# Kernel tuning notes

Measured on AMD Instinct MI355X. Metric: run time of the kernel, lower is better.

## Reference

```python
import jax, jax.numpy as jnp
import numpy as np

B, N, E, H, MAXLEN = 64, 256, 1024, 16, 512
D = E // H
LN_EPS = 1e-5
NORM_EPS = 1e-12


def setup_inputs() -> dict:
    key = jax.random.key(0)
    ks = jax.random.split(key, 12)
    s = 1.0 / np.sqrt(E)
    return {
        "news_embeds": jax.random.normal(ks[0], (B, N, E), jnp.float32),
        "padding_mask": jax.random.uniform(ks[1], (B, N)) > 0.8,  # True = padded
        "cls_token": jax.random.normal(ks[2], (1, 1, E), jnp.float32),
        "pos_emb": jax.random.normal(ks[3], (MAXLEN + 1, E), jnp.float32) * 0.02,
        "in_proj_w": jax.random.normal(ks[4], (3 * E, E), jnp.float32) * s,
        "in_proj_b": jnp.zeros((3 * E,), jnp.float32),
        "out_proj_w": jax.random.normal(ks[5], (E, E), jnp.float32) * s,
        "out_proj_b": jnp.zeros((E,), jnp.float32),
        "proj_w": jax.random.normal(ks[6], (E, E), jnp.float32) * s,
        "proj_b": jnp.zeros((E,), jnp.float32),
        "ln_gamma": jnp.ones((E,), jnp.float32),
        "ln_beta": jnp.zeros((E,), jnp.float32),
    }


def reference(news_embeds, padding_mask, cls_token, pos_emb, in_proj_w, in_proj_b,
              out_proj_w, out_proj_b, proj_w, proj_b, ln_gamma, ln_beta):
    b, n, e = news_embeds.shape
    S = n + 1
    # prepend CLS token, add positional encodings (dropout inactive in eval)
    x = jnp.concatenate([jnp.broadcast_to(cls_token, (b, 1, e)), news_embeds], axis=1)
    x = x + pos_emb[:S][None, :, :]
    # key padding mask with CLS always attendable
    mask = jnp.concatenate(
        [jnp.zeros((b, 1), dtype=bool), padding_mask], axis=1)  # [b,S]
    # packed QKV projection (nn.MultiheadAttention in_proj)
    qkv = jnp.einsum('bse,fe->bsf', x, in_proj_w) + in_proj_b
    q, k, v = jnp.split(qkv, 3, axis=-1)
    q = q.reshape(b, S, H, D)
    k = k.reshape(b, S, H, D)
    v = v.reshape(b, S, H, D)
    scores = jnp.einsum('bqhd,bkhd->bhqk', q, k) / jnp.sqrt(
        jnp.asarray(D, x.dtype))
    big_neg = jnp.asarray(-1e9, scores.dtype)
    scores = jnp.where(mask[:, None, None, :], big_neg, scores)
    attn = jax.nn.softmax(scores, axis=-1)  # [b,H,S,S]
    ctx = jnp.einsum('bhqk,bkhd->bqhd', attn, v).reshape(b, S, e)
    attn_out = jnp.einsum('bse,fe->bsf', ctx, out_proj_w) + out_proj_b
    # projection head: Linear -> (Dropout eval noop) -> LayerNorm -> ReLU
    p = jnp.einsum('bse,fe->bsf', attn_out, proj_w) + proj_b
    mu = jnp.mean(p, axis=-1, keepdims=True)
    var = jnp.var(p, axis=-1, keepdims=True)
    ln = (p - mu) * jax.lax.rsqrt(var + LN_EPS) * ln_gamma + ln_beta
    proj = jax.nn.relu(ln)
    user = proj[:, 0, :]
    norm = jnp.maximum(jnp.linalg.norm(user, axis=-1, keepdims=True), NORM_EPS)
    user = user / norm
    return user, attn
```

## Files before the change

kernel.cpp:

```cpp
#include <hip/hip_runtime.h>

#define B_   64
#define N_   256
#define E_   1024
#define H_   16
#define D_   64
#define S_   257
#define M_   16448
#define MP2  16640
#define N3_  3072
#define K_   1024

typedef unsigned short u16;
typedef unsigned int   u32;
typedef __bf16 bf16x8 __attribute__((ext_vector_type(8)));
typedef float  f32x4  __attribute__((ext_vector_type(4)));

__device__ inline u16 f2bf(float f) {
  union { float f; u32 u; } a; a.f = f;
  return (u16)((a.u + 0x7FFFu + ((a.u >> 16) & 1u)) >> 16);
}
__device__ inline float bf2f(u16 h) {
  union { u32 u; float f; } a; a.u = ((u32)h) << 16; return a.f;
}
__device__ inline void gload_lds16(const void* g, void* l) {
  __builtin_amdgcn_global_load_lds((const __attribute__((address_space(1))) void*)g,
                                   (__attribute__((address_space(3))) void*)l, 16, 0, 0);
}

__global__ __launch_bounds__(256) void prep_w(const float* __restrict__ w, u16* __restrict__ o) {
  size_t i = ((size_t)blockIdx.x * 256 + threadIdx.x) * 4;
  float4 f = *(const float4*)(w + i);
  ushort4 v;
  v.x = f2bf(f.x); v.y = f2bf(f.y); v.z = f2bf(f.z); v.w = f2bf(f.w);
  *(ushort4*)(o + i) = v;
}

__global__ __launch_bounds__(256) void build_x(const float* __restrict__ news,
                                               const float* __restrict__ cls,
                                               const float* __restrict__ pos,
                                               u16* __restrict__ x) {
  const int row = blockIdx.x;
  const int e = threadIdx.x * 4;
  float4 v = make_float4(0.f, 0.f, 0.f, 0.f);
  if (row < M_) {
    const int b = row / S_;
    const int s = row - b * S_;
    float4 pe = *(const float4*)(pos + (size_t)s * E_ + e);
    float4 xv = (s == 0) ? *(const float4*)(cls + e)
                         : *(const float4*)(news + ((size_t)b * N_ + (s - 1)) * E_ + e);
    v.x = xv.x + pe.x; v.y = xv.y + pe.y; v.z = xv.z + pe.z; v.w = xv.w + pe.w;
  }
  ushort4 o;
  o.x = f2bf(v.x); o.y = f2bf(v.y); o.z = f2bf(v.z); o.w = f2bf(v.w);
  *(ushort4*)(x + (size_t)row * E_ + e) = o;
}

__global__ __launch_bounds__(256) void mask_prep(const void* __restrict__ src, int* __restrict__ dst) {
  const int t = threadIdx.x;
  const u32* wsrc = (const u32*)src;
  u32 flag = 0;
  for (int i = t; i < 4096; i += 256) {
    u32 v = wsrc[i];
    if (v == 0x3F800000u) flag |= 2u;
    else if (v > 1u) flag |= 1u;
  }
  __shared__ u32 fsh;
  if (t == 0) fsh = 0;
  __syncthreads();
  if (flag) atomicOr(&fsh, flag);
  __syncthreads();
  const u32 f = fsh;
  const int mode = (f & 2u) ? 2 : ((f & 1u) ? 1 : 0);
  const int base = blockIdx.x * 2048;
  for (int i = base + t; i < base + 2048; i += 256) {
    int m;
    if (mode == 0)      m = (wsrc[i] != 0u);
    else if (mode == 2) m = (((const float*)src)[i] != 0.f);
    else                m = (((const unsigned char*)src)[i] != 0);
    dst[i] = m;
  }
}

__global__ __launch_bounds__(256) void gemm_qkv(const u16* __restrict__ A,
                                                const u16* __restrict__ Bw,
                                                const float* __restrict__ bias,
                                                u16* __restrict__ C) {
  __shared__ u16 As[128 * 32];
  __shared__ u16 Bs[128 * 32];
  const int t = threadIdx.x;
  const int w = t >> 6, l = t & 63;
  const int wr = w >> 1, wc = w & 1;

  const int orig = blockIdx.x;
  const int wgid = (orig & 7) * 390 + (orig >> 3);
  const int bm = wgid / 24, bn = wgid % 24;

  const u16* Ab = A + (size_t)bm * 128 * K_;
  const u16* Bb = Bw + (size_t)bn * 128 * K_;
  f32x4 acc[4][4] = {};
  const int r0 = t >> 2,         col0 = (t & 3) << 3;
  const int r1 = (256 + t) >> 2, col1 = ((256 + t) & 3) << 3;
  char* AsB = (char*)As + w * 1024;
  char* BsB = (char*)Bs + w * 1024;

  for (int k0 = 0; k0 < K_; k0 += 32) {
    gload_lds16(Ab + (size_t)r0 * K_ + k0 + col0, AsB);
    gload_lds16(Ab + (size_t)r1 * K_ + k0 + col1, AsB + 4096);
    gload_lds16(Bb + (size_t)r0 * K_ + k0 + col0, BsB);
    gload_lds16(Bb + (size_t)r1 * K_ + k0 + col1, BsB + 4096);
    __syncthreads();
    const int kc = (l >> 4) << 3;
    bf16x8 af[4], bfr[4];
#pragma unroll
    for (int m = 0; m < 4; ++m)
      af[m] = *(const bf16x8*)&As[(wr * 64 + m * 16 + (l & 15)) * 32 + kc];
#pragma unroll
    for (int n = 0; n < 4; ++n)
      bfr[n] = *(const bf16x8*)&Bs[(wc * 64 + n * 16 + (l & 15)) * 32 + kc];
#pragma unroll
    for (int m = 0; m < 4; ++m)
#pragma unroll
      for (int n = 0; n < 4; ++n)
        acc[m][n] = __builtin_amdgcn_mfma_f32_16x16x32_bf16(af[m], bfr[n], acc[m][n], 0, 0, 0);
    __syncthreads();
  }
  const int row0 = bm * 128 + wr * 64 + ((l >> 4) << 2);
  const int colb = bn * 128 + wc * 64 + (l & 15);
#pragma unroll
  for (int n = 0; n < 4; ++n) {
    const int col = colb + n * 16;
    const float bv = bias[col];
#pragma unroll
    for (int m = 0; m < 4; ++m) {
      const int row = row0 + m * 16;
#pragma unroll
      for (int j = 0; j < 4; ++j)
        C[(size_t)(row + j) * N3_ + col] = f2bf(acc[m][n][j] + bv);
    }
  }
}

__global__ __launch_bounds__(256) void attn_kernel(const u16* __restrict__ qkv,
                                                   const int* __restrict__ maskw,
                                                   float* __restrict__ attn,
                                                   float* __restrict__ ctx) {
  __shared__ u16 Ks[258 * 72];
  __shared__ float msk[272];
  __shared__ float p0[272];
  __shared__ float red[4][64];
  const int qt = blockIdx.x, h = blockIdx.y, b = blockIdx.z;
  const int t = threadIdx.x;
  const int q0 = qt * 64;

  for (int c = t; c < 258 * 8; c += 256) {
    const int r = c >> 3, qq = c & 7;
    uint4 val = make_uint4(0, 0, 0, 0);
    if (r < S_)
      val = *(const uint4*)(qkv + (size_t)(b * S_ + r) * N3_ + E_ + h * 64 + qq * 8);
    *(uint4*)&Ks[r * 72 + qq * 8] = val;
  }
  for (int i = t; i < 272; i += 256) {
    float m = 0.f;
    if (i == 0) m = 1.f;
    else if (i < S_) m = maskw[b * N_ + i - 1] ? 0.f : 1.f;
    msk[i] = m;
  }
  __syncthreads();

  const int w = t >> 6, l = t & 63;
  const int cl = l & 15, rg = l >> 4;
  const int kc = rg * 8;

  const u16* qrow = qkv + (size_t)(b * S_ + q0 + w * 16 + cl) * N3_ + h * 64 + kc;
  const bf16x8 qa0 = *(const bf16x8*)qrow;
  const bf16x8 qa1 = *(const bf16x8*)(qrow + 32);

#define QK(kt, a)                                                                  \
  {                                                                                \
    int krow = (kt) * 16 + cl;                                                     \
    if (krow > 257) krow = 257;                                                    \
    const u16* kb = &Ks[krow * 72 + kc];                                           \
    (a) = __builtin_amdgcn_mfma_f32_16x16x32_bf16(qa0, *(const bf16x8*)kb, (a), 0, 0, 0); \
    (a) = __builtin_amdgcn_mfma_f32_16x16x32_bf16(qa1, *(const bf16x8*)(kb + 32), (a), 0, 0, 0); \
  }

  float sum[4] = {0.f, 0.f, 0.f, 0.f};
#pragma unroll
  for (int kt = 0; kt < 17; ++kt) {
    f32x4 a = {0.f, 0.f, 0.f, 0.f};
    QK(kt, a);
    const float m = msk[kt * 16 + cl];
#pragma unroll
    for (int j = 0; j < 4; ++j)
      sum[j] += m * __expf(a[j] * 0.125f);
  }
  float inv[4];
#pragma unroll
  for (int j = 0; j < 4; ++j) {
#pragma unroll
    for (int o = 1; o < 16; o <<= 1) sum[j] += __shfl_xor(sum[j], o);
    inv[j] = 1.f / sum[j];
  }

  const int qrow0 = q0 + w * 16 + rg * 4;
  float* abase = attn + (size_t)(b * H_ + h) * S_ * S_;
  float* arow[4];
  bool okq[4];
#pragma unroll
  for (int j = 0; j < 4; ++j) {
    const int gq = qrow0 + j;
    okq[j] = (gq < S_);
    arow[j] = abase + (size_t)gq * S_;
  }
  const bool isCls = (qt == 0 && w == 0 && rg == 0);
#pragma unroll
  for (int kt = 0; kt < 17; ++kt) {
    f32x4 a = {0.f, 0.f, 0.f, 0.f};
    QK(kt, a);
    const float m = msk[kt * 16 + cl];
    const int col = kt * 16 + cl;
    const bool okc = (col < S_);
#pragma unroll
    for (int j = 0; j < 4; ++j) {
      const float v = m * __expf(a[j] * 0.125f) * inv[j];
      if (okc && okq[j]) arow[j][col] = v;
      if (isCls && j == 0) p0[col] = v;
    }
  }
#undef QK

  if (qt == 0) {
    __syncthreads();
    const int part = t >> 6, d = t & 63;
    float acc = 0.f;
    for (int k = part; k < S_; k += 4)
      acc = fmaf(p0[k], bf2f(qkv[(size_t)(b * S_ + k) * N3_ + 2 * E_ + h * 64 + d]), acc);
    red[part][d] = acc;
    __syncthreads();
    if (t < 64)
      ctx[(size_t)b * E_ + h * 64 + t] = red[0][t] + red[1][t] + red[2][t] + red[3][t];
  }
}

__global__ __launch_bounds__(256) void gemv_cls(const float* __restrict__ in,
                                                const float* __restrict__ W,
                                                const float* __restrict__ bias,
                                                float* __restrict__ out) {
  const int bt = blockIdx.x, fc = blockIdx.y, t = threadIdx.x;
  __shared__ float xs[4][E_];
  for (int i = t; i < E_; i += 256)
    ((float4*)xs)[i] = ((const float4*)(in + (size_t)bt * 4 * E_))[i];
  __syncthreads();
  const int f = fc * 64 + (t >> 2);
  const int ec = (t & 3) * 256;
  const float4* wr = (const float4*)(W + (size_t)f * E_ + ec);
  float a0 = 0.f, a1 = 0.f, a2 = 0.f, a3 = 0.f;
#pragma unroll 8
  for (int e4 = 0; e4 < 64; ++e4) {
    const float4 wv = wr[e4];
    const float4 x0 = *(const float4*)&xs[0][ec + e4 * 4];
    const float4 x1 = *(const float4*)&xs[1][ec + e4 * 4];
    const float4 x2 = *(const float4*)&xs[2][ec + e4 * 4];
    const float4 x3 = *(const float4*)&xs[3][ec + e4 * 4];
    a0 += wv.x * x0.x + wv.y * x0.y + wv.z * x0.z + wv.w * x0.w;
    a1 += wv.x * x1.x + wv.y * x1.y + wv.z * x1.z + wv.w * x1.w;
    a2 += wv.x * x2.x + wv.y * x2.y + wv.z * x2.z + wv.w * x2.w;
    a3 += wv.x * x3.x + wv.y * x3.y + wv.z * x3.z + wv.w * x3.w;
  }
  a0 += __shfl_xor(a0, 1); a0 += __shfl_xor(a0, 2);
  a1 += __shfl_xor(a1, 1); a1 += __shfl_xor(a1, 2);
  a2 += __shfl_xor(a2, 1); a2 += __shfl_xor(a2, 2);
  a3 += __shfl_xor(a3, 1); a3 += __shfl_xor(a3, 2);
  if ((t & 3) == 0) {
    const float bv = bias[f];
    out[(size_t)(bt * 4 + 0) * E_ + f] = a0 + bv;
    out[(size_t)(bt * 4 + 1) * E_ + f] = a1 + bv;
    out[(size_t)(bt * 4 + 2) * E_ + f] = a2 + bv;
    out[(size_t)(bt * 4 + 3) * E_ + f] = a3 + bv;
  }
}

__global__ __launch_bounds__(256) void ln_relu_norm(const float* __restrict__ p,
                                                    const float* __restrict__ gamma,
                                                    const float* __restrict__ beta,
                                                    float* __restrict__ user) {
  const int b = blockIdx.x, t = threadIdx.x;
  const int w = t >> 6, l = t & 63;
  const float4 v = ((const float4*)(p + (size_t)b * E_))[t];
  float s = v.x + v.y + v.z + v.w;
  float s2 = v.x * v.x + v.y * v.y + v.z * v.z + v.w * v.w;
#pragma unroll
  for (int o = 1; o < 64; o <<= 1) { s += __shfl_xor(s, o); s2 += __shfl_xor(s2, o); }
  __shared__ float ss[4], ss2[4], qs[4];
  if (l == 0) { ss[w] = s; ss2[w] = s2; }
  __syncthreads();
  s = ss[0] + ss[1] + ss[2] + ss[3];
  s2 = ss2[0] + ss2[1] + ss2[2] + ss2[3];
  const float mu = s * (1.f / E_);
  const float var = s2 * (1.f / E_) - mu * mu;
  const float rstd = rsqrtf(var + 1e-5f);
  const float4 g = ((const float4*)gamma)[t];
  const float4 be = ((const float4*)beta)[t];
  float4 o;
  o.x = fmaxf((v.x - mu) * rstd * g.x + be.x, 0.f);
  o.y = fmaxf((v.y - mu) * rstd * g.y + be.y, 0.f);
  o.z = fmaxf((v.z - mu) * rstd * g.z + be.z, 0.f);
  o.w = fmaxf((v.w - mu) * rstd * g.w + be.w, 0.f);
  float q2 = o.x * o.x + o.y * o.y + o.z * o.z + o.w * o.w;
#pragma unroll
  for (int off = 1; off < 64; off <<= 1) q2 += __shfl_xor(q2, off);
  if (l == 0) qs[w] = q2;
  __syncthreads();
  q2 = qs[0] + qs[1] + qs[2] + qs[3];
  const float nrm = fmaxf(sqrtf(q2), 1e-12f);
  const float inv = 1.f / nrm;
  float4 u;
  u.x = o.x * inv; u.y = o.y * inv; u.z = o.z * inv; u.w = o.w * inv;
  ((float4*)(user + (size_t)b * E_))[t] = u;
}

extern "C" void kernel_launch(void* const* d_in, const int* in_sizes, int n_in,
                              void* d_out, int out_size, void* d_ws, size_t ws_size,
                              hipStream_t stream) {
  const float* news   = (const float*)d_in[0];
  const void*  maskp  = d_in[1];
  const float* cls    = (const float*)d_in[2];
  const float* pos    = (const float*)d_in[3];
  const float* w_in   = (const float*)d_in[4];
  const float* b_in   = (const float*)d_in[5];
  const float* w_out  = (const float*)d_in[6];
  const float* b_out  = (const float*)d_in[7];
  const float* w_proj = (const float*)d_in[8];
  const float* b_proj = (const float*)d_in[9];
  const float* gamma  = (const float*)d_in[10];
  const float* beta   = (const float*)d_in[11];

  char* ws = (char*)d_ws;
  u16*  w_bf  = (u16*)(ws + 0);
  u16*  x_bf  = (u16*)(ws + 6291456);
  u16*  qkv   = (u16*)(ws + 40370176);
  float* ctx  = (float*)(ws + 142606336);
  float* aoc  = (float*)(ws + 142868480);
  float* pcls = (float*)(ws + 143130624);
  int*  maskw = (int*)(ws + 143392768);

  float* user = (float*)d_out;
  float* attn = (float*)d_out + (size_t)B_ * E_;

  prep_w<<<3072, 256, 0, stream>>>(w_in, w_bf);
  build_x<<<MP2, 256, 0, stream>>>(news, cls, pos, x_bf);
  mask_prep<<<8, 256, 0, stream>>>(maskp, maskw);
  gemm_qkv<<<3120, 256, 0, stream>>>(x_bf, w_bf, b_in, qkv);
  attn_kernel<<<dim3(5, H_, B_), 256, 0, stream>>>(qkv, maskw, attn, ctx);
  gemv_cls<<<dim3(16, 16), 256, 0, stream>>>(ctx, w_out, b_out, aoc);
  gemv_cls<<<dim3(16, 16), 256, 0, stream>>>(aoc, w_proj, b_proj, pcls);
  ln_relu_norm<<<B_, 256, 0, stream>>>(pcls, gamma, beta, user);
}
```

Measured before the change: 357.8 us.

## Use fragment-ordered LDS staging in QKV GEMM and transpose attention score MFMA

The QKV GEMM now stages 64-wide K slices per barrier, laid out in LDS so each lane reads its MFMA fragment contiguously. This halves the barrier count and avoids bank conflicts. The attention kernel swaps the MFMA operands so each lane holds four consecutive key columns of one query row. That reduces the row-sum to two shuffles and allows 16-byte vector stores of attention probabilities instead of scattered scalar stores. The stores are only 4-byte aligned because S=257 is odd, so memcpy may split them, and the doubled LDS footprint may lower occupancy.

```diff
diff --git a/kernel.cpp b/kernel.cpp
--- a/kernel.cpp
+++ b/kernel.cpp
@@ -86,8 +86,8 @@
                                                 const u16* __restrict__ Bw,
                                                 const float* __restrict__ bias,
                                                 u16* __restrict__ C) {
-  __shared__ u16 As[128 * 32];
-  __shared__ u16 Bs[128 * 32];
+  __shared__ u16 ldsA[8192];
+  __shared__ u16 ldsB[8192];
   const int t = threadIdx.x;
   const int w = t >> 6, l = t & 63;
   const int wr = w >> 1, wc = w & 1;
@@ -96,35 +96,45 @@
   const int wgid = (orig & 7) * 390 + (orig >> 3);
   const int bm = wgid / 24, bn = wgid % 24;
 
-  const u16* Ab = A + (size_t)bm * 128 * K_;
-  const u16* Bb = Bw + (size_t)bn * 128 * K_;
+  const u16* Abase = A + (size_t)bm * 128 * K_;
+  const u16* Bbase = Bw + (size_t)bn * 128 * K_;
+
   f32x4 acc[4][4] = {};
-  const int r0 = t >> 2,         col0 = (t & 3) << 3;
-  const int r1 = (256 + t) >> 2, col1 = ((256 + t) & 3) << 3;
-  char* AsB = (char*)As + w * 1024;
-  char* BsB = (char*)Bs + w * 1024;
-
-  for (int k0 = 0; k0 < K_; k0 += 32) {
-    gload_lds16(Ab + (size_t)r0 * K_ + k0 + col0, AsB);
-    gload_lds16(Ab + (size_t)r1 * K_ + k0 + col1, AsB + 4096);
-    gload_lds16(Bb + (size_t)r0 * K_ + k0 + col0, BsB);
-    gload_lds16(Bb + (size_t)r1 * K_ + k0 + col1, BsB + 4096);
+
+#define STAGE(k0)                                                                 \
+  {                                                                               \
+    _Pragma("unroll")                                                             \
+    for (int c = 0; c < 4; ++c) {                                                 \
+      const int bi = w * 4 + c;                                                   \
+      const size_t off = (size_t)((bi >> 1) * 16 + (l & 15)) * K_ +               \
+                         (bi & 1) * 32 + ((l >> 4) * 8) + (k0);                   \
+      gload_lds16(Abase + off, (char*)ldsA + bi * 1024);                          \
+      gload_lds16(Bbase + off, (char*)ldsB + bi * 1024);                          \
+    }                                                                             \
+  }
+
+  for (int kt = 0; kt < 16; ++kt) {
+    STAGE(kt * 64);
     __syncthreads();
-    const int kc = (l >> 4) << 3;
-    bf16x8 af[4], bfr[4];
-#pragma unroll
-    for (int m = 0; m < 4; ++m)
-      af[m] = *(const bf16x8*)&As[(wr * 64 + m * 16 + (l & 15)) * 32 + kc];
-#pragma unroll
-    for (int n = 0; n < 4; ++n)
-      bfr[n] = *(const bf16x8*)&Bs[(wc * 64 + n * 16 + (l & 15)) * 32 + kc];
-#pragma unroll
-    for (int m = 0; m < 4; ++m)
+#pragma unroll
+    for (int half = 0; half < 2; ++half) {
+      bf16x8 af[4], bfx[4];
+#pragma unroll
+      for (int m = 0; m < 4; ++m)
+        af[m] = *(const bf16x8*)&ldsA[(((wr * 4 + m) * 2 + half) * 64 + l) * 8];
 #pragma unroll
       for (int n = 0; n < 4; ++n)
-        acc[m][n] = __builtin_amdgcn_mfma_f32_16x16x32_bf16(af[m], bfr[n], acc[m][n], 0, 0, 0);
+        bfx[n] = *(const bf16x8*)&ldsB[(((wc * 4 + n) * 2 + half) * 64 + l) * 8];
+#pragma unroll
+      for (int m = 0; m < 4; ++m)
+#pragma unroll
+        for (int n = 0; n < 4; ++n)
+          acc[m][n] = __builtin_amdgcn_mfma_f32_16x16x32_bf16(af[m], bfx[n], acc[m][n], 0, 0, 0);
+    }
     __syncthreads();
   }
+#undef STAGE
+
   const int row0 = bm * 128 + wr * 64 + ((l >> 4) << 2);
   const int colb = bn * 128 + wc * 64 + (l & 15);
 #pragma unroll
@@ -173,59 +183,52 @@
   const int kc = rg * 8;
 
   const u16* qrow = qkv + (size_t)(b * S_ + q0 + w * 16 + cl) * N3_ + h * 64 + kc;
-  const bf16x8 qa0 = *(const bf16x8*)qrow;
-  const bf16x8 qa1 = *(const bf16x8*)(qrow + 32);
+  const bf16x8 qb0 = *(const bf16x8*)qrow;
+  const bf16x8 qb1 = *(const bf16x8*)(qrow + 32);
 
 #define QK(kt, a)                                                                  \
   {                                                                                \
     int krow = (kt) * 16 + cl;                                                     \
     if (krow > 257) krow = 257;                                                    \
     const u16* kb = &Ks[krow * 72 + kc];                                           \
-    (a) = __builtin_amdgcn_mfma_f32_16x16x32_bf16(qa0, *(const bf16x8*)kb, (a), 0, 0, 0); \
-    (a) = __builtin_amdgcn_mfma_f32_16x16x32_bf16(qa1, *(const bf16x8*)(kb + 32), (a), 0, 0, 0); \
-  }
-
-  float sum[4] = {0.f, 0.f, 0.f, 0.f};
+    (a) = __builtin_amdgcn_mfma_f32_16x16x32_bf16(*(const bf16x8*)kb, qb0, (a), 0, 0, 0); \
+    (a) = __builtin_amdgcn_mfma_f32_16x16x32_bf16(*(const bf16x8*)(kb + 32), qb1, (a), 0, 0, 0); \
+  }
+
+  float sum = 0.f;
 #pragma unroll
   for (int kt = 0; kt < 17; ++kt) {
     f32x4 a = {0.f, 0.f, 0.f, 0.f};
     QK(kt, a);
-    const float m = msk[kt * 16 + cl];
+    const f32x4 m4 = *(const f32x4*)&msk[kt * 16 + rg * 4];
 #pragma unroll
     for (int j = 0; j < 4; ++j)
-      sum[j] += m * __expf(a[j] * 0.125f);
-  }
-  float inv[4];
-#pragma unroll
-  for (int j = 0; j < 4; ++j) {
-#pragma unroll
-    for (int o = 1; o < 16; o <<= 1) sum[j] += __shfl_xor(sum[j], o);
-    inv[j] = 1.f / sum[j];
-  }
-
-  const int qrow0 = q0 + w * 16 + rg * 4;
-  float* abase = attn + (size_t)(b * H_ + h) * S_ * S_;
-  float* arow[4];
-  bool okq[4];
-#pragma unroll
-  for (int j = 0; j < 4; ++j) {
-    const int gq = qrow0 + j;
-    okq[j] = (gq < S_);
-    arow[j] = abase + (size_t)gq * S_;
-  }
-  const bool isCls = (qt == 0 && w == 0 && rg == 0);
+      sum += m4[j] * __expf(a[j] * 0.125f);
+  }
+  sum += __shfl_xor(sum, 16);
+  sum += __shfl_xor(sum, 32);
+  const float inv = 1.f / sum;
+
+  const int gq = q0 + w * 16 + cl;
+  const bool ok = (gq < S_);
+  float* arow = attn + (size_t)((b * H_ + h) * S_ + gq) * S_;
+  const bool isCls = (qt == 0 && w == 0 && cl == 0);
 #pragma unroll
   for (int kt = 0; kt < 17; ++kt) {
     f32x4 a = {0.f, 0.f, 0.f, 0.f};
     QK(kt, a);
-    const float m = msk[kt * 16 + cl];
-    const int col = kt * 16 + cl;
-    const bool okc = (col < S_);
-#pragma unroll
-    for (int j = 0; j < 4; ++j) {
-      const float v = m * __expf(a[j] * 0.125f) * inv[j];
-      if (okc && okq[j]) arow[j][col] = v;
-      if (isCls && j == 0) p0[col] = v;
+    const f32x4 m4 = *(const f32x4*)&msk[kt * 16 + rg * 4];
+    f32x4 v;
+#pragma unroll
+    for (int j = 0; j < 4; ++j)
+      v[j] = m4[j] * __expf(a[j] * 0.125f) * inv;
+    if (ok) {
+      if (kt < 16)       __builtin_memcpy(arow + kt * 16 + rg * 4, &v, 16);
+      else if (rg == 0)  arow[256] = v[0];
+    }
+    if (isCls) {
+#pragma unroll
+      for (int j = 0; j < 4; ++j) p0[kt * 16 + rg * 4 + j] = v[j];
     }
   }
 #undef QK
```

Result: slower. 436.5 us (+22.0%).
